# Kernel tuning notes

Measured on AMD Instinct MI355X. Metric: run time of the kernel, lower is better.

The kernel has to match this reference:

```python
import jax, jax.numpy as jnp
import numpy as np
import math

B, C, N = 8, 512, 2048

def setup_inputs() -> dict:
    key = jax.random.key(0)
    ks = jax.random.split(key, 7)
    s = 0.02
    return {
        "x": jax.random.normal(ks[0], (B, C, N), dtype=jnp.float32),
        "Wq": jax.random.normal(ks[1], (C // 2, C), dtype=jnp.float32) * s,
        "bq": jax.random.normal(ks[2], (C // 2,), dtype=jnp.float32) * s,
        "Wk": jax.random.normal(ks[3], (C // 2, C), dtype=jnp.float32) * s,
        "bk": jax.random.normal(ks[4], (C // 2,), dtype=jnp.float32) * s,
        "Wv": jax.random.normal(ks[5], (C, C), dtype=jnp.float32) * s,
        "bv": jax.random.normal(ks[6], (C,), dtype=jnp.float32) * s,
    }

def reference(x, Wq, bq, Wk, bk, Wv, bv):
    # pointwise conv1d == channel matmul: (O,C) x (B,C,N) -> (B,O,N)
    Q = jnp.einsum('oc,bcn->bon', Wq, x) + bq[None, :, None]  # (B, C/2, N)
    K = jnp.einsum('oc,bcn->bon', Wk, x) + bk[None, :, None]  # (B, C/2, N)
    V = jnp.einsum('oc,bcn->bon', Wv, x) + bv[None, :, None]  # (B, C, N)
    scale = 1.0 / math.sqrt(K.shape[1])
    A = jnp.einsum('bcn,bcm->bnm', Q, K) * scale              # (B, N, N)
    A = jax.nn.softmax(A, axis=-1)
    out = jnp.einsum('bcm,bnm->bcn', V, A)                    # V @ A^T
    return x + out
```

## Files before the change

### kernel.cpp

```cpp
#include <hip/hip_runtime.h>

#define B_ 8
#define C_ 512
#define N_ 2048
#define O_ 256

typedef unsigned short u16;
typedef unsigned char u8;
typedef unsigned int uint;
typedef __bf16 bf16x8 __attribute__((ext_vector_type(8)));
typedef float f32x4 __attribute__((ext_vector_type(4)));
typedef int i32x8 __attribute__((ext_vector_type(8)));

#define AS1 __attribute__((address_space(1)))
#define AS3 __attribute__((address_space(3)))

__device__ __forceinline__ u16 f2bf(float f) {
  union { float f; unsigned u; } v; v.f = f;
  return (u16)((v.u + 0x7fffu + ((v.u >> 16) & 1u)) >> 16);
}

__device__ __forceinline__ uint pk4_e4m3(float a, float b, float c, float d) {
  int r = __builtin_amdgcn_cvt_pk_fp8_f32(a, b, 0, false);
  r = __builtin_amdgcn_cvt_pk_fp8_f32(c, d, r, true);
  return (uint)r;
}

__device__ __forceinline__ void mfma_mainloop(
    const u16* __restrict__ Ag, int lda,
    const u16* __restrict__ Bg, int ldb, int K,
    u16 (&As)[128][64], u16 (&Bs)[128][64], f32x4 (&acc)[4][4])
{
  const int t = threadIdx.x;
  const int lane = t & 63;
  const int w = t >> 6;
  const int wm = (w >> 1) * 64, wn = (w & 1) * 64;
  const int lrow = lane & 15, quad = lane >> 4;
  const int r8 = lane >> 3;
  const int kgsrc = (lane & 7) ^ r8;
  const int swz = lrow & 7;

  for (int k0 = 0; k0 < K; k0 += 64) {
#pragma unroll
    for (int i = 0; i < 4; i++) {
      int row = w * 32 + i * 8;
      __builtin_amdgcn_global_load_lds(
          (const AS1 uint*)(Ag + (size_t)(row + r8) * lda + k0 + kgsrc * 8),
          (AS3 uint*)(&As[row][0]), 16, 0, 0);
      __builtin_amdgcn_global_load_lds(
          (const AS1 uint*)(Bg + (size_t)(row + r8) * ldb + k0 + kgsrc * 8),
          (AS3 uint*)(&Bs[row][0]), 16, 0, 0);
    }
    __syncthreads();
#pragma unroll
    for (int kk = 0; kk < 2; kk++) {
      const int pg = (kk * 4 + quad) ^ swz;
      bf16x8 af[4], bfr[4];
#pragma unroll
      for (int i = 0; i < 4; i++)
        af[i] = *(const bf16x8*)(&As[wm + i * 16 + lrow][pg * 8]);
#pragma unroll
      for (int j = 0; j < 4; j++)
        bfr[j] = *(const bf16x8*)(&Bs[wn + j * 16 + lrow][pg * 8]);
#pragma unroll
      for (int i = 0; i < 4; i++)
#pragma unroll
        for (int j = 0; j < 4; j++)
          acc[i][j] = __builtin_amdgcn_mfma_f32_16x16x32_bf16(af[i], bfr[j], acc[i][j], 0, 0, 0);
    }
    __syncthreads();
  }
}

__global__ __launch_bounds__(256) void convert_w_kernel(
    const float* __restrict__ Wq, const float* __restrict__ Wk,
    const float* __restrict__ Wv,
    u16* __restrict__ Wqb, u16* __restrict__ Wkb, u16* __restrict__ Wvb)
{
  int i = blockIdx.x * 256 + threadIdx.x;
  if (i < O_ * C_) { Wqb[i] = f2bf(Wq[i]); Wkb[i] = f2bf(Wk[i]); }
  Wvb[i] = f2bf(Wv[i]);
}

__global__ __launch_bounds__(256) void transpose_kernel(
    const float* __restrict__ x, u16* __restrict__ xT)
{
  __shared__ u16 tile[64][72];
  int b = blockIdx.z;
  int n0 = blockIdx.x * 64, c0 = blockIdx.y * 64;
  int t = threadIdx.x;
  const float* src = x + (size_t)b * C_ * N_ + (size_t)c0 * N_ + n0;
  int r = t >> 4;
  int f4 = (t & 15) * 4;
#pragma unroll
  for (int i = 0; i < 4; i++) {
    int c = r + 16 * i;
    float4 v = *(const float4*)(src + (size_t)c * N_ + f4);
    tile[f4 + 0][c] = f2bf(v.x);
    tile[f4 + 1][c] = f2bf(v.y);
    tile[f4 + 2][c] = f2bf(v.z);
    tile[f4 + 3][c] = f2bf(v.w);
  }
  __syncthreads();
  u16* dst = xT + (size_t)b * N_ * C_ + (size_t)n0 * C_ + c0;
  int nr = t >> 3;
  int cc = (t & 7) * 8;
#pragma unroll
  for (int i = 0; i < 2; i++) {
    int n = nr + 32 * i;
    *(uint4*)(dst + (size_t)n * C_ + cc) = *(const uint4*)(&tile[n][cc]);
  }
}

__global__ __launch_bounds__(256) void proj_qk_kernel(
    const u16* __restrict__ xT, const u16* __restrict__ Wqb, const float* __restrict__ bq,
    const u16* __restrict__ Wkb, const float* __restrict__ bk,
    u16* __restrict__ Qt, u16* __restrict__ Kt)
{
  __shared__ u16 As[128][64], Bs[128][64];
  int b = blockIdx.z >> 1, isK = blockIdx.z & 1;
  int n0 = blockIdx.y * 128, o0 = blockIdx.x * 128;
  const u16* Ag = xT + (size_t)b * N_ * C_ + (size_t)n0 * C_;
  const u16* Bg = (isK ? Wkb : Wqb) + (size_t)o0 * C_;
  const float* bias = isK ? bk : bq;
  u16* outp = (isK ? Kt : Qt) + (size_t)b * N_ * O_;

  const f32x4 zero = {0.f, 0.f, 0.f, 0.f};
  f32x4 acc[4][4];
#pragma unroll
  for (int i = 0; i < 4; i++)
#pragma unroll
    for (int j = 0; j < 4; j++) acc[i][j] = zero;

  mfma_mainloop(Ag, C_, Bg, C_, C_, As, Bs, acc);

  const int lane = threadIdx.x & 63;
  const int w = threadIdx.x >> 6;
  const int wm = (w >> 1) * 64, wn = (w & 1) * 64;
  const int quad = lane >> 4, lcol = lane & 15;
#pragma unroll
  for (int j = 0; j < 4; j++) {
    int o = o0 + wn + j * 16 + lcol;
    float bb = bias[o];
#pragma unroll
    for (int i = 0; i < 4; i++)
#pragma unroll
      for (int rr = 0; rr < 4; rr++) {
        int n = n0 + wm + i * 16 + quad * 4 + rr;
        outp[(size_t)n * O_ + o] = f2bf(acc[i][j][rr] + bb);
      }
  }
}

__global__ __launch_bounds__(256) void proj_v_kernel(
    const u16* __restrict__ xT, const u16* __restrict__ Wvb, const float* __restrict__ bv,
    u8* __restrict__ V)
{
  __shared__ u16 As[128][64], Bs[128][64];
  int b = blockIdx.z;
  int c0 = blockIdx.y * 128, n0 = blockIdx.x * 128;
  const u16* Ag = xT + (size_t)b * N_ * C_ + (size_t)n0 * C_;
  const u16* Bg = Wvb + (size_t)c0 * C_;
  u8* outp = V + (size_t)b * C_ * N_;

  const f32x4 zero = {0.f, 0.f, 0.f, 0.f};
  f32x4 acc[4][4];
#pragma unroll
  for (int i = 0; i < 4; i++)
#pragma unroll
    for (int j = 0; j < 4; j++) acc[i][j] = zero;

  mfma_mainloop(Ag, C_, Bg, C_, C_, As, Bs, acc);

  const int lane = threadIdx.x & 63;
  const int w = threadIdx.x >> 6;
  const int wm = (w >> 1) * 64, wn = (w & 1) * 64;
  const int quad = lane >> 4, lcol = lane & 15;
#pragma unroll
  for (int j = 0; j < 4; j++) {
    int c = c0 + wn + j * 16 + lcol;
    float bb = bv[c];
#pragma unroll
    for (int i = 0; i < 4; i++) {
      int nbase = n0 + wm + i * 16 + quad * 4;
      uint d = pk4_e4m3(acc[i][j][0] + bb, acc[i][j][1] + bb,
                        acc[i][j][2] + bb, acc[i][j][3] + bb);
      *(uint*)(outp + (size_t)c * N_ + nbase) = d;
    }
  }
}

__global__ __launch_bounds__(256) void attn_s_kernel(
    const u16* __restrict__ Qt, const u16* __restrict__ Kt,
    u8* __restrict__ P, float* __restrict__ rowsum)
{
  __shared__ u16 As[128][64], Bs[128][64];
  int b = blockIdx.z;
  int m0 = blockIdx.x * 128, n0 = blockIdx.y * 128;
  const u16* Ag = Kt + (size_t)b * N_ * O_ + (size_t)m0 * O_;
  const u16* Bg = Qt + (size_t)b * N_ * O_ + (size_t)n0 * O_;

  const f32x4 zero = {0.f, 0.f, 0.f, 0.f};
  f32x4 acc[4][4];
#pragma unroll
  for (int i = 0; i < 4; i++)
#pragma unroll
    for (int j = 0; j < 4; j++) acc[i][j] = zero;

  mfma_mainloop(Ag, O_, Bg, O_, O_, As, Bs, acc);

  u8* Pp = P + (size_t)b * N_ * N_;
  float* rs = rowsum + (size_t)b * N_;
  const int lane = threadIdx.x & 63;
  const int w = threadIdx.x >> 6;
  const int wm = (w >> 1) * 64, wn = (w & 1) * 64;
  const int quad = lane >> 4, lcol = lane & 15;

  float partial[4];
#pragma unroll
  for (int j = 0; j < 4; j++) partial[j] = 0.f;

#pragma unroll
  for (int j = 0; j < 4; j++) {
    int n = n0 + wn + j * 16 + lcol;
#pragma unroll
    for (int i = 0; i < 4; i++) {
      int mbase = m0 + wm + i * 16 + quad * 4;
      float p0 = __expf(acc[i][j][0] * 0.0625f);
      float p1 = __expf(acc[i][j][1] * 0.0625f);
      float p2 = __expf(acc[i][j][2] * 0.0625f);
      float p3 = __expf(acc[i][j][3] * 0.0625f);
      *(uint*)(Pp + (size_t)n * N_ + mbase) = pk4_e4m3(p0, p1, p2, p3);
      partial[j] += p0 + p1 + p2 + p3;
    }
  }
#pragma unroll
  for (int msk = 16; msk < 64; msk <<= 1)
#pragma unroll
    for (int j = 0; j < 4; j++)
      partial[j] += __shfl_xor(partial[j], msk);
  if (quad == 0) {
#pragma unroll
    for (int j = 0; j < 4; j++)
      atomicAdd(&rs[n0 + wn + j * 16 + lcol], partial[j]);
  }
}

__global__ __launch_bounds__(256) void attn_o_kernel(
    const u8* __restrict__ V, const u8* __restrict__ P,
    const float* __restrict__ rowsum, const float* __restrict__ x,
    float* __restrict__ out)
{
  __shared__ __align__(16) u8 As[128][128], Bs[128][128];
  int b = blockIdx.z;
  int c0 = blockIdx.y * 128, n0 = blockIdx.x * 128;
  const u8* Ag = V + (size_t)b * C_ * N_ + (size_t)c0 * N_;
  const u8* Bg = P + (size_t)b * N_ * N_ + (size_t)n0 * N_;

  const int t = threadIdx.x;
  const int lane = t & 63;
  const int w = t >> 6;
  const int wm = (w >> 1) * 64, wn = (w & 1) * 64;
  const int lrow = lane & 15, quad = lane >> 4;
  const int swz = lrow & 7;
  const int r8 = lane >> 3;
  const int gsrc = (lane & 7) ^ r8;

  const f32x4 zero = {0.f, 0.f, 0.f, 0.f};
  f32x4 acc[4][4];
#pragma unroll
  for (int i = 0; i < 4; i++)
#pragma unroll
    for (int j = 0; j < 4; j++) acc[i][j] = zero;

  union Frag { i32x8 v; uint4 q[2]; };

  for (int k0 = 0; k0 < N_; k0 += 128) {
#pragma unroll
    for (int i = 0; i < 4; i++) {
      int row = i * 32 + w * 8;
      __builtin_amdgcn_global_load_lds(
          (const AS1 uint*)(Ag + (size_t)(row + r8) * N_ + k0 + gsrc * 16),
          (AS3 uint*)(&As[row][0]), 16, 0, 0);
      __builtin_amdgcn_global_load_lds(
          (const AS1 uint*)(Bg + (size_t)(row + r8) * N_ + k0 + gsrc * 16),
          (AS3 uint*)(&Bs[row][0]), 16, 0, 0);
    }
    __syncthreads();
    const int g0 = (quad * 2) ^ swz, g1 = (quad * 2 + 1) ^ swz;
    Frag af[4], bfr[4];
#pragma unroll
    for (int i = 0; i < 4; i++) {
      const u8* rp = &As[wm + i * 16 + lrow][0];
      af[i].q[0] = *(const uint4*)(rp + g0 * 16);
      af[i].q[1] = *(const uint4*)(rp + g1 * 16);
    }
#pragma unroll
    for (int j = 0; j < 4; j++) {
      const u8* rp = &Bs[wn + j * 16 + lrow][0];
      bfr[j].q[0] = *(const uint4*)(rp + g0 * 16);
      bfr[j].q[1] = *(const uint4*)(rp + g1 * 16);
    }
#pragma unroll
    for (int i = 0; i < 4; i++)
#pragma unroll
      for (int j = 0; j < 4; j++)
        acc[i][j] = __builtin_amdgcn_mfma_scale_f32_16x16x128_f8f6f4(
            af[i].v, bfr[j].v, acc[i][j],
            0, 0,
            0, 0x7f7f7f7f,
            0, 0x7f7f7f7f);
    __syncthreads();
  }

  const float* xb = x + (size_t)b * C_ * N_;
  float* ob = out + (size_t)b * C_ * N_;
  float invl[4];
#pragma unroll
  for (int j = 0; j < 4; j++)
    invl[j] = 1.f / rowsum[b * N_ + n0 + wn + j * 16 + lrow];

#pragma unroll
  for (int i = 0; i < 4; i++)
#pragma unroll
    for (int rr = 0; rr < 4; rr++) {
      int c = c0 + wm + i * 16 + quad * 4 + rr;
#pragma unroll
      for (int j = 0; j < 4; j++) {
        int n = n0 + wn + j * 16 + lrow;
        size_t idx = (size_t)c * N_ + n;
        ob[idx] = xb[idx] + acc[i][j][rr] * invl[j];
      }
    }
}

extern "C" void kernel_launch(void* const* d_in, const int* in_sizes, int n_in,
                              void* d_out, int out_size, void* d_ws, size_t ws_size,
                              hipStream_t stream)
{
  (void)in_sizes; (void)n_in; (void)out_size; (void)ws_size;
  const float* x  = (const float*)d_in[0];
  const float* Wq = (const float*)d_in[1];
  const float* bq = (const float*)d_in[2];
  const float* Wk = (const float*)d_in[3];
  const float* bk = (const float*)d_in[4];
  const float* Wv = (const float*)d_in[5];
  const float* bv = (const float*)d_in[6];
  float* out = (float*)d_out;

  char* ws = (char*)d_ws;
  size_t off = 0;
  auto carve = [&](size_t bytes) -> char* {
    char* p = ws + off;
    off += (bytes + 255) & ~(size_t)255;
    return p;
  };
  u16* xT   = (u16*)carve((size_t)B_ * N_ * C_ * 2);
  u16* Wqb  = (u16*)carve((size_t)O_ * C_ * 2);
  u16* Wkb  = (u16*)carve((size_t)O_ * C_ * 2);
  u16* Wvb  = (u16*)carve((size_t)C_ * C_ * 2);
  u16* Qt   = (u16*)carve((size_t)B_ * N_ * O_ * 2);
  u16* Kt   = (u16*)carve((size_t)B_ * N_ * O_ * 2);
  u8*  Vb   = (u8*) carve((size_t)B_ * C_ * N_);
  u8*  P    = (u8*) carve((size_t)B_ * N_ * N_);
  float* rowsum = (float*)carve((size_t)B_ * N_ * 4);

  hipMemsetAsync(rowsum, 0, (size_t)B_ * N_ * 4, stream);
  convert_w_kernel<<<dim3((C_ * C_) / 256), 256, 0, stream>>>(Wq, Wk, Wv, Wqb, Wkb, Wvb);
  transpose_kernel<<<dim3(N_ / 64, C_ / 64, B_), 256, 0, stream>>>(x, xT);
  proj_qk_kernel<<<dim3(O_ / 128, N_ / 128, B_ * 2), 256, 0, stream>>>(xT, Wqb, bq, Wkb, bk, Qt, Kt);
  proj_v_kernel<<<dim3(N_ / 128, C_ / 128, B_), 256, 0, stream>>>(xT, Wvb, bv, Vb);
  attn_s_kernel<<<dim3(N_ / 128, N_ / 128, B_), 256, 0, stream>>>(Qt, Kt, P, rowsum);
  attn_o_kernel<<<dim3(N_ / 128, C_ / 128, B_), 256, 0, stream>>>(Vb, P, rowsum, x, out);
}
```

Baseline: 194.0 us.

## Quantize Q/K to fp8 for MX score GEMM and merge projection kernels

Q and K projections now emit fp8 e4m3 instead of bf16, and the score GEMM switches to the scaled fp8 MFMA mainloop shared with the output GEMM. The Q, K and V projections are merged into a single launch, and the rowsum memset is folded into the weight-conversion kernel. This halves Q/K traffic, doubles MFMA throughput in the score stage and removes two launches. In exchange, attention logits lose precision, which risks accuracy.

```diff
diff --git a/kernel.cpp b/kernel.cpp
--- a/kernel.cpp
+++ b/kernel.cpp
@@ -72,14 +72,71 @@
   }
 }
 
+union MxFrag { i32x8 v; uint4 q[2]; };
+
+__device__ __forceinline__ void mx_mainloop(
+    const u8* __restrict__ Ag, int lda,
+    const u8* __restrict__ Bg, int ldb, int K,
+    u8 (&As)[128][128], u8 (&Bs)[128][128], f32x4 (&acc)[4][4])
+{
+  const int t = threadIdx.x;
+  const int lane = t & 63;
+  const int w = t >> 6;
+  const int wm = (w >> 1) * 64, wn = (w & 1) * 64;
+  const int lrow = lane & 15, quad = lane >> 4;
+  const int swz = lrow & 7;
+  const int r8 = lane >> 3;
+  const int gsrc = (lane & 7) ^ r8;
+
+  for (int k0 = 0; k0 < K; k0 += 128) {
+#pragma unroll
+    for (int i = 0; i < 4; i++) {
+      int row = i * 32 + w * 8;
+      __builtin_amdgcn_global_load_lds(
+          (const AS1 uint*)(Ag + (size_t)(row + r8) * lda + k0 + gsrc * 16),
+          (AS3 uint*)(&As[row][0]), 16, 0, 0);
+      __builtin_amdgcn_global_load_lds(
+          (const AS1 uint*)(Bg + (size_t)(row + r8) * ldb + k0 + gsrc * 16),
+          (AS3 uint*)(&Bs[row][0]), 16, 0, 0);
+    }
+    __syncthreads();
+    const int g0 = (quad * 2) ^ swz, g1 = (quad * 2 + 1) ^ swz;
+    MxFrag af[4], bfr[4];
+#pragma unroll
+    for (int i = 0; i < 4; i++) {
+      const u8* rp = &As[wm + i * 16 + lrow][0];
+      af[i].q[0] = *(const uint4*)(rp + g0 * 16);
+      af[i].q[1] = *(const uint4*)(rp + g1 * 16);
+    }
+#pragma unroll
+    for (int j = 0; j < 4; j++) {
+      const u8* rp = &Bs[wn + j * 16 + lrow][0];
+      bfr[j].q[0] = *(const uint4*)(rp + g0 * 16);
+      bfr[j].q[1] = *(const uint4*)(rp + g1 * 16);
+    }
+#pragma unroll
+    for (int i = 0; i < 4; i++)
+#pragma unroll
+      for (int j = 0; j < 4; j++)
+        acc[i][j] = __builtin_amdgcn_mfma_scale_f32_16x16x128_f8f6f4(
+            af[i].v, bfr[j].v, acc[i][j],
+            0, 0,
+            0, 0x7f7f7f7f,
+            0, 0x7f7f7f7f);
+    __syncthreads();
+  }
+}
+
 __global__ __launch_bounds__(256) void convert_w_kernel(
     const float* __restrict__ Wq, const float* __restrict__ Wk,
     const float* __restrict__ Wv,
-    u16* __restrict__ Wqb, u16* __restrict__ Wkb, u16* __restrict__ Wvb)
+    u16* __restrict__ Wqb, u16* __restrict__ Wkb, u16* __restrict__ Wvb,
+    float* __restrict__ rowsum)
 {
   int i = blockIdx.x * 256 + threadIdx.x;
   if (i < O_ * C_) { Wqb[i] = f2bf(Wq[i]); Wkb[i] = f2bf(Wk[i]); }
   Wvb[i] = f2bf(Wv[i]);
+  if (i < B_ * N_) rowsum[i] = 0.f;
 }
 
 __global__ __launch_bounds__(256) void transpose_kernel(
@@ -112,18 +169,18 @@
   }
 }
 
-__global__ __launch_bounds__(256) void proj_qk_kernel(
-    const u16* __restrict__ xT, const u16* __restrict__ Wqb, const float* __restrict__ bq,
+__global__ __launch_bounds__(256) void proj_all_kernel(
+    const u16* __restrict__ xT,
+    const u16* __restrict__ Wqb, const float* __restrict__ bq,
     const u16* __restrict__ Wkb, const float* __restrict__ bk,
-    u16* __restrict__ Qt, u16* __restrict__ Kt)
+    const u16* __restrict__ Wvb, const float* __restrict__ bv,
+    u8* __restrict__ Qt8, u8* __restrict__ Kt8, u8* __restrict__ V8)
 {
   __shared__ u16 As[128][64], Bs[128][64];
-  int b = blockIdx.z >> 1, isK = blockIdx.z & 1;
-  int n0 = blockIdx.y * 128, o0 = blockIdx.x * 128;
-  const u16* Ag = xT + (size_t)b * N_ * C_ + (size_t)n0 * C_;
-  const u16* Bg = (isK ? Wkb : Wqb) + (size_t)o0 * C_;
-  const float* bias = isK ? bk : bq;
-  u16* outp = (isK ? Kt : Qt) + (size_t)b * N_ * O_;
+  const int n0 = blockIdx.x * 128;
+  const int b = blockIdx.y;
+  const int sub = blockIdx.z;
+  const u16* xTb = xT + (size_t)b * N_ * C_ + (size_t)n0 * C_;
 
   const f32x4 zero = {0.f, 0.f, 0.f, 0.f};
   f32x4 acc[4][4];
@@ -132,36 +189,63 @@
 #pragma unroll
     for (int j = 0; j < 4; j++) acc[i][j] = zero;
 
-  mfma_mainloop(Ag, C_, Bg, C_, C_, As, Bs, acc);
-
   const int lane = threadIdx.x & 63;
   const int w = threadIdx.x >> 6;
   const int wm = (w >> 1) * 64, wn = (w & 1) * 64;
   const int quad = lane >> 4, lcol = lane & 15;
-#pragma unroll
-  for (int j = 0; j < 4; j++) {
-    int o = o0 + wn + j * 16 + lcol;
-    float bb = bias[o];
-#pragma unroll
-    for (int i = 0; i < 4; i++)
-#pragma unroll
-      for (int rr = 0; rr < 4; rr++) {
-        int n = n0 + wm + i * 16 + quad * 4 + rr;
-        outp[(size_t)n * O_ + o] = f2bf(acc[i][j][rr] + bb);
+
+  if (sub < 4) {
+    const int isK = sub >> 1;
+    const int o0 = (sub & 1) * 128;
+    const u16* Wg = (isK ? Wkb : Wqb) + (size_t)o0 * C_;
+    const float* bias = isK ? bk : bq;
+    u8* outp = (isK ? Kt8 : Qt8) + (size_t)b * N_ * O_;
+
+    mfma_mainloop(Wg, C_, xTb, C_, C_, As, Bs, acc);
+
+#pragma unroll
+    for (int i = 0; i < 4; i++) {
+      int obase = o0 + wm + i * 16 + quad * 4;
+      float4 bb = *(const float4*)(bias + obase);
+#pragma unroll
+      for (int j = 0; j < 4; j++) {
+        int n = n0 + wn + j * 16 + lcol;
+        uint d = pk4_e4m3(acc[i][j][0] + bb.x, acc[i][j][1] + bb.y,
+                          acc[i][j][2] + bb.z, acc[i][j][3] + bb.w);
+        *(uint*)(outp + (size_t)n * O_ + obase) = d;
       }
-  }
-}
-
-__global__ __launch_bounds__(256) void proj_v_kernel(
-    const u16* __restrict__ xT, const u16* __restrict__ Wvb, const float* __restrict__ bv,
-    u8* __restrict__ V)
-{
-  __shared__ u16 As[128][64], Bs[128][64];
+    }
+  } else {
+    const int c0 = (sub - 4) * 128;
+    const u16* Wg = Wvb + (size_t)c0 * C_;
+    u8* outp = V8 + (size_t)b * C_ * N_;
+
+    mfma_mainloop(xTb, C_, Wg, C_, C_, As, Bs, acc);
+
+#pragma unroll
+    for (int j = 0; j < 4; j++) {
+      int c = c0 + wn + j * 16 + lcol;
+      float bb = bv[c];
+#pragma unroll
+      for (int i = 0; i < 4; i++) {
+        int nbase = n0 + wm + i * 16 + quad * 4;
+        uint d = pk4_e4m3(acc[i][j][0] + bb, acc[i][j][1] + bb,
+                          acc[i][j][2] + bb, acc[i][j][3] + bb);
+        *(uint*)(outp + (size_t)c * N_ + nbase) = d;
+      }
+    }
+  }
+}
+
+__global__ __launch_bounds__(256) void attn_s_kernel(
+    const u8* __restrict__ Qt8, const u8* __restrict__ Kt8,
+    u8* __restrict__ P, float* __restrict__ rowsum)
+{
+  __shared__ __align__(16) u8 As[128][128], Bs[128][128];
   int b = blockIdx.z;
-  int c0 = blockIdx.y * 128, n0 = blockIdx.x * 128;
-  const u16* Ag = xT + (size_t)b * N_ * C_ + (size_t)n0 * C_;
-  const u16* Bg = Wvb + (size_t)c0 * C_;
-  u8* outp = V + (size_t)b * C_ * N_;
+  int m0 = blockIdx.x * 128, n0 = blockIdx.y * 128;
+  const u8* Ag = Kt8 + (size_t)b * N_ * O_ + (size_t)m0 * O_;
+  const u8* Bg = Qt8 + (size_t)b * N_ * O_ + (size_t)n0 * O_;
 
   const f32x4 zero = {0.f, 0.f, 0.f, 0.f};
   f32x4 acc[4][4];
@@ -170,44 +254,7 @@
 #pragma unroll
     for (int j = 0; j < 4; j++) acc[i][j] = zero;
 
-  mfma_mainloop(Ag, C_, Bg, C_, C_, As, Bs, acc);
-
-  const int lane = threadIdx.x & 63;
-  const int w = threadIdx.x >> 6;
-  const int wm = (w >> 1) * 64, wn = (w & 1) * 64;
-  const int quad = lane >> 4, lcol = lane & 15;
-#pragma unroll
-  for (int j = 0; j < 4; j++) {
-    int c = c0 + wn + j * 16 + lcol;
-    float bb = bv[c];
-#pragma unroll
-    for (int i = 0; i < 4; i++) {
-      int nbase = n0 + wm + i * 16 + quad * 4;
-      uint d = pk4_e4m3(acc[i][j][0] + bb, acc[i][j][1] + bb,
-                        acc[i][j][2] + bb, acc[i][j][3] + bb);
-      *(uint*)(outp + (size_t)c * N_ + nbase) = d;
-    }
-  }
-}
-
-__global__ __launch_bounds__(256) void attn_s_kernel(
-    const u16* __restrict__ Qt, const u16* __restrict__ Kt,
-    u8* __restrict__ P, float* __restrict__ rowsum)
-{
-  __shared__ u16 As[128][64], Bs[128][64];
-  int b = blockIdx.z;
-  int m0 = blockIdx.x * 128, n0 = blockIdx.y * 128;
-  const u16* Ag = Kt + (size_t)b * N_ * O_ + (size_t)m0 * O_;
-  const u16* Bg = Qt + (size_t)b * N_ * O_ + (size_t)n0 * O_;
-
-  const f32x4 zero = {0.f, 0.f, 0.f, 0.f};
-  f32x4 acc[4][4];
-#pragma unroll
-  for (int i = 0; i < 4; i++)
-#pragma unroll
-    for (int j = 0; j < 4; j++) acc[i][j] = zero;
-
-  mfma_mainloop(Ag, O_, Bg, O_, O_, As, Bs, acc);
+  mx_mainloop(Ag, O_, Bg, O_, O_, As, Bs, acc);
 
   u8* Pp = P + (size_t)b * N_ * N_;
   float* rs = rowsum + (size_t)b * N_;
@@ -257,15 +304,6 @@
   const u8* Ag = V + (size_t)b * C_ * N_ + (size_t)c0 * N_;
   const u8* Bg = P + (size_t)b * N_ * N_ + (size_t)n0 * N_;
 
-  const int t = threadIdx.x;
-  const int lane = t & 63;
-  const int w = t >> 6;
-  const int wm = (w >> 1) * 64, wn = (w & 1) * 64;
-  const int lrow = lane & 15, quad = lane >> 4;
-  const int swz = lrow & 7;
-  const int r8 = lane >> 3;
-  const int gsrc = (lane & 7) ^ r8;
-
   const f32x4 zero = {0.f, 0.f, 0.f, 0.f};
   f32x4 acc[4][4];
 #pragma unroll
@@ -273,45 +311,12 @@
 #pragma unroll
     for (int j = 0; j < 4; j++) acc[i][j] = zero;
 
-  union Frag { i32x8 v; uint4 q[2]; };
-
-  for (int k0 = 0; k0 < N_; k0 += 128) {
-#pragma unroll
-    for (int i = 0; i < 4; i++) {
-      int row = i * 32 + w * 8;
-      __builtin_amdgcn_global_load_lds(
-          (const AS1 uint*)(Ag + (size_t)(row + r8) * N_ + k0 + gsrc * 16),
-          (AS3 uint*)(&As[row][0]), 16, 0, 0);
-      __builtin_amdgcn_global_load_lds(
-          (const AS1 uint*)(Bg + (size_t)(row + r8) * N_ + k0 + gsrc * 16),
-          (AS3 uint*)(&Bs[row][0]), 16, 0, 0);
-    }
-    __syncthreads();
-    const int g0 = (quad * 2) ^ swz, g1 = (quad * 2 + 1) ^ swz;
-    Frag af[4], bfr[4];
-#pragma unroll
-    for (int i = 0; i < 4; i++) {
-      const u8* rp = &As[wm + i * 16 + lrow][0];
-      af[i].q[0] = *(const uint4*)(rp + g0 * 16);
-      af[i].q[1] = *(const uint4*)(rp + g1 * 16);
-    }
-#pragma unroll
-    for (int j = 0; j < 4; j++) {
-      const u8* rp = &Bs[wn + j * 16 + lrow][0];
-      bfr[j].q[0] = *(const uint4*)(rp + g0 * 16);
-      bfr[j].q[1] = *(const uint4*)(rp + g1 * 16);
-    }
-#pragma unroll
-    for (int i = 0; i < 4; i++)
-#pragma unroll
-      for (int j = 0; j < 4; j++)
-        acc[i][j] = __builtin_amdgcn_mfma_scale_f32_16x16x128_f8f6f4(
-            af[i].v, bfr[j].v, acc[i][j],
-            0, 0,
-            0, 0x7f7f7f7f,
-            0, 0x7f7f7f7f);
-    __syncthreads();
-  }
+  mx_mainloop(Ag, N_, Bg, N_, N_, As, Bs, acc);
+
+  const int lane = threadIdx.x & 63;
+  const int w = threadIdx.x >> 6;
+  const int wm = (w >> 1) * 64, wn = (w & 1) * 64;
+  const int quad = lane >> 4, lrow = lane & 15;
 
   const float* xb = x + (size_t)b * C_ * N_;
   float* ob = out + (size_t)b * C_ * N_;
@@ -359,17 +364,17 @@
   u16* Wqb  = (u16*)carve((size_t)O_ * C_ * 2);
   u16* Wkb  = (u16*)carve((size_t)O_ * C_ * 2);
   u16* Wvb  = (u16*)carve((size_t)C_ * C_ * 2);
-  u16* Qt   = (u16*)carve((size_t)B_ * N_ * O_ * 2);
-  u16* Kt   = (u16*)carve((size_t)B_ * N_ * O_ * 2);
+  u8*  Qt8  = (u8*) carve((size_t)B_ * N_ * O_);
+  u8*  Kt8  = (u8*) carve((size_t)B_ * N_ * O_);
   u8*  Vb   = (u8*) carve((size_t)B_ * C_ * N_);
   u8*  P    = (u8*) carve((size_t)B_ * N_ * N_);
   float* rowsum = (float*)carve((size_t)B_ * N_ * 4);
 
-  hipMemsetAsync(rowsum, 0, (size_t)B_ * N_ * 4, stream);
-  convert_w_kernel<<<dim3((C_ * C_) / 256), 256, 0, stream>>>(Wq, Wk, Wv, Wqb, Wkb, Wvb);
+  convert_w_kernel<<<dim3((C_ * C_) / 256), 256, 0, stream>>>(
+      Wq, Wk, Wv, Wqb, Wkb, Wvb, rowsum);
   transpose_kernel<<<dim3(N_ / 64, C_ / 64, B_), 256, 0, stream>>>(x, xT);
-  proj_qk_kernel<<<dim3(O_ / 128, N_ / 128, B_ * 2), 256, 0, stream>>>(xT, Wqb, bq, Wkb, bk, Qt, Kt);
-  proj_v_kernel<<<dim3(N_ / 128, C_ / 128, B_), 256, 0, stream>>>(xT, Wvb, bv, Vb);
-  attn_s_kernel<<<dim3(N_ / 128, N_ / 128, B_), 256, 0, stream>>>(Qt, Kt, P, rowsum);
+  proj_all_kernel<<<dim3(N_ / 128, B_, 8), 256, 0, stream>>>(
+      xT, Wqb, bq, Wkb, bk, Wvb, bv, Qt8, Kt8, Vb);
+  attn_s_kernel<<<dim3(N_ / 128, N_ / 128, B_), 256, 0, stream>>>(Qt8, Kt8, P, rowsum);
   attn_o_kernel<<<dim3(N_ / 128, C_ / 128, B_), 256, 0, stream>>>(Vb, P, rowsum, x, out);
 }
```

New measurement: 179.8 us. -7.4%, faster.
